# Kernel optimization log

Measured on AMD Instinct MI355X. Metric: run time of the kernel, lower is better.

Reference implementation:

```python
import jax, jax.numpy as jnp
import numpy as np

NUM_CLASSES = 150
EPS = 1e-8


def _class_centers(features, labels):
    # features: [B, Cf, H, W] float; labels: [B, H, W] int
    # Single-pass segment reduce over pixels keyed by class label, replacing the
    # original O(C*N) per-class masked passes.
    B, Cf, H, W = features.shape
    f = features.reshape(B, Cf, H * W)          # [B, Cf, N]
    l = labels.reshape(B, H * W)                # [B, N]

    def per_batch(fb, lb):
        # fb: [Cf, N], lb: [N]
        sums = jax.ops.segment_sum(fb.T, lb, num_segments=NUM_CLASSES)      # [C, Cf]
        counts = jax.ops.segment_sum(jnp.ones_like(lb, fb.dtype), lb,
                                      num_segments=NUM_CLASSES)             # [C]
        return sums / (counts[:, None] + EPS)                               # [C, Cf]

    centers = jax.vmap(per_batch)(f, l)         # [B, C, Cf]
    return centers.mean(axis=0)                 # [C, Cf]


def setup_inputs() -> dict:
    key = jax.random.key(0)
    k1, k2, k3, k4 = jax.random.split(key, 4)
    B, Cf, H, W = 1, 256, 512, 512
    return {
        "src_fea": jax.random.normal(k1, (B, Cf, H, W), dtype=jnp.float32),
        "trg_fea": jax.random.normal(k2, (B, Cf, H, W), dtype=jnp.float32),
        "src_labels": jax.random.randint(k3, (B, H, W), 0, NUM_CLASSES, dtype=jnp.int32),
        "trg_pseudo_labels": jax.random.randint(k4, (B, H, W), 0, NUM_CLASSES, dtype=jnp.int32),
    }


def reference(src_fea, trg_fea, src_labels, trg_pseudo_labels):
    cs = _class_centers(src_fea, src_labels)                # [C, Cf]
    ct = _class_centers(trg_fea, trg_pseudo_labels)         # [C, Cf]
    return jnp.linalg.norm(cs - ct)                         # scalar Frobenius norm
```

## Files before the change

kernel.cpp:

```cpp
#include <hip/hip_runtime.h>
#include <math.h>

#define N_PIX (512 * 512)
#define NQ (N_PIX / 4)
#define NUM_CLASSES 150
#define CF 256
#define ACC_STRIDE 151
#define DUMP 150
#define PIX_PER_BLOCK 2048
#define QUADS_PER_BLOCK (PIX_PER_BLOCK / 4)
#define CHUNKS (N_PIX / PIX_PER_BLOCK)
#define THREADS 256
#define EPS 1e-8f


__device__ __forceinline__ void rmw_quad(float* __restrict__ arow, float4 v,
                                         int4 L) {
  float vx = v.x, vy = v.y, vz = v.z, vw = v.w;
  int ax = L.x, ay = L.y, az = L.z, aw = L.w;
  if (L.y == L.x) { vx += vy; ay = DUMP; }
  if (L.z == L.x) { vx += vz; az = DUMP; }
  else if (L.z == L.y) { vy += vz; az = DUMP; }
  if (L.w == L.x) { vx += vw; aw = DUMP; }
  else if (L.w == L.y) { vy += vw; aw = DUMP; }
  else if (L.w == L.z) { vz += vw; aw = DUMP; }
  const float r0 = arow[ax];
  const float r1 = arow[ay];
  const float r2 = arow[az];
  const float r3 = arow[aw];
  arow[ax] = r0 + vx;
  arow[ay] = r1 + vy;
  arow[az] = r2 + vz;
  arow[aw] = r3 + vw;
}

__global__ __launch_bounds__(THREADS, 1) void scatter_kernel(
    const float* __restrict__ f_src, const float* __restrict__ f_trg,
    const int* __restrict__ l_src, const int* __restrict__ l_trg,
    float* __restrict__ sums, float* __restrict__ cnt) {
  const int tensor = blockIdx.z;
  const float* __restrict__ f = tensor ? f_trg : f_src;
  const int* __restrict__ lab = tensor ? l_trg : l_src;

  __shared__ float acc[CF * ACC_STRIDE];

  const int t = threadIdx.x;
  for (int i = t; i < CF * ACC_STRIDE; i += THREADS) acc[i] = 0.f;
  __syncthreads();

  const int q0 = blockIdx.x * QUADS_PER_BLOCK;
  const float4* __restrict__ fb4 = (const float4*)f + (size_t)t * NQ;
  const int4* __restrict__ lab4 = (const int4*)lab;
  float* __restrict__ arow = &acc[t * ACC_STRIDE];

  int my_count = 0;

  int q = q0;
  float4 a0 = fb4[q + 0], a1 = fb4[q + 1], a2 = fb4[q + 2], a3 = fb4[q + 3];
  int4 b0 = lab4[q + 0], b1 = lab4[q + 1], b2 = lab4[q + 2], b3 = lab4[q + 3];

  for (int j = 0; j < QUADS_PER_BLOCK; j += 4) {
    const float4 v0 = a0, v1 = a1, v2 = a2, v3 = a3;
    const int4 L0 = b0, L1 = b1, L2 = b2, L3 = b3;
    q = q0 + ((j + 4) & (QUADS_PER_BLOCK - 1));
    a0 = fb4[q + 0]; a1 = fb4[q + 1]; a2 = fb4[q + 2]; a3 = fb4[q + 3];
    b0 = lab4[q + 0]; b1 = lab4[q + 1]; b2 = lab4[q + 2]; b3 = lab4[q + 3];

    my_count += (L0.x == t) + (L0.y == t) + (L0.z == t) + (L0.w == t) +
                (L1.x == t) + (L1.y == t) + (L1.z == t) + (L1.w == t) +
                (L2.x == t) + (L2.y == t) + (L2.z == t) + (L2.w == t) +
                (L3.x == t) + (L3.y == t) + (L3.z == t) + (L3.w == t);

    rmw_quad(arow, v0, L0);
    rmw_quad(arow, v1, L1);
    rmw_quad(arow, v2, L2);
    rmw_quad(arow, v3, L3);
  }
  __syncthreads();

  float* __restrict__ out = sums + tensor * (NUM_CLASSES * CF);
  for (int i = t; i < NUM_CLASSES * CF; i += THREADS) {
    const int cls = i >> 8;
    const int ch = i & (CF - 1);
    unsafeAtomicAdd(&out[i], acc[ch * ACC_STRIDE + cls]);
  }
  if (t < NUM_CLASSES)
    unsafeAtomicAdd(&cnt[tensor * NUM_CLASSES + t], (float)my_count);
}

#define FTHREADS 1024
__global__ __launch_bounds__(FTHREADS) void finalize_kernel(
    const float* __restrict__ sums, const float* __restrict__ cnt,
    float* __restrict__ out) {
  const float* ss = sums;
  const float* st = sums + NUM_CLASSES * CF;
  const float* cs = cnt;
  const float* ct = cnt + NUM_CLASSES;
  float acc = 0.f;
  for (int i = threadIdx.x; i < NUM_CLASSES * CF; i += FTHREADS) {
    const int cls = i >> 8;
    const float d = ss[i] / (cs[cls] + EPS) - st[i] / (ct[cls] + EPS);
    acc += d * d;
  }
#pragma unroll
  for (int off = 32; off > 0; off >>= 1) acc += __shfl_down(acc, off, 64);
  __shared__ float red[FTHREADS / 64];
  const int lane = threadIdx.x & 63;
  const int wid = threadIdx.x >> 6;
  if (lane == 0) red[wid] = acc;
  __syncthreads();
  if (threadIdx.x == 0) {
    float tsum = 0.f;
#pragma unroll
    for (int w = 0; w < FTHREADS / 64; ++w) tsum += red[w];
    out[0] = sqrtf(tsum);
  }
}

extern "C" void kernel_launch(void* const* d_in, const int* in_sizes, int n_in,
                              void* d_out, int out_size, void* d_ws,
                              size_t ws_size, hipStream_t stream) {
  const float* f_src = (const float*)d_in[0];
  const float* f_trg = (const float*)d_in[1];
  const int* l_src = (const int*)d_in[2];
  const int* l_trg = (const int*)d_in[3];
  float* out = (float*)d_out;

  float* sums = (float*)d_ws;
  float* cnt = sums + 2 * NUM_CLASSES * CF;

  const size_t zero_bytes =
      (size_t)(2 * NUM_CLASSES * CF + 2 * NUM_CLASSES) * sizeof(float);
  hipMemsetAsync(d_ws, 0, zero_bytes, stream);

  hipLaunchKernelGGL(scatter_kernel, dim3(CHUNKS, 1, 2), dim3(THREADS), 0,
                     stream, f_src, f_trg, l_src, l_trg, sums, cnt);
  hipLaunchKernelGGL(finalize_kernel, dim3(1), dim3(FTHREADS), 0, stream, sums,
                     cnt, out);
}
```

Baseline: 615.4 us.

## Stage packed labels in shared memory and double-buffer deeper feature prefetch

Labels for the block are loaded once cooperatively, packed into bytes, and stored in shared memory instead of every thread re-reading the same int4 labels from global memory. Feature loads are now double-buffered in batches of 16 float4s per thread, which raises memory-level parallelism to hide global latency in the scatter loop. This costs more registers (32 float4 buffers) and a small extra LDS array, and packing assumes labels fit in 8 bits.

```diff
diff --git a/kernel.cpp b/kernel.cpp
--- a/kernel.cpp
+++ b/kernel.cpp
@@ -11,19 +11,20 @@
 #define QUADS_PER_BLOCK (PIX_PER_BLOCK / 4)
 #define CHUNKS (N_PIX / PIX_PER_BLOCK)
 #define THREADS 256
+#define BATCH 16
 #define EPS 1e-8f
 
 
 __device__ __forceinline__ void rmw_quad(float* __restrict__ arow, float4 v,
-                                         int4 L) {
+                                         int lx, int ly, int lz, int lw) {
   float vx = v.x, vy = v.y, vz = v.z, vw = v.w;
-  int ax = L.x, ay = L.y, az = L.z, aw = L.w;
-  if (L.y == L.x) { vx += vy; ay = DUMP; }
-  if (L.z == L.x) { vx += vz; az = DUMP; }
-  else if (L.z == L.y) { vy += vz; az = DUMP; }
-  if (L.w == L.x) { vx += vw; aw = DUMP; }
-  else if (L.w == L.y) { vy += vw; aw = DUMP; }
-  else if (L.w == L.z) { vz += vw; aw = DUMP; }
+  int ax = lx, ay = ly, az = lz, aw = lw;
+  if (ly == lx) { vx += vy; ay = DUMP; }
+  if (lz == lx) { vx += vz; az = DUMP; }
+  else if (lz == ly) { vy += vz; az = DUMP; }
+  if (lw == lx) { vx += vw; aw = DUMP; }
+  else if (lw == ly) { vy += vw; aw = DUMP; }
+  else if (lw == lz) { vz += vw; aw = DUMP; }
   const float r0 = arow[ax];
   const float r1 = arow[ay];
   const float r2 = arow[az];
@@ -43,39 +44,50 @@
   const int* __restrict__ lab = tensor ? l_trg : l_src;
 
   __shared__ float acc[CF * ACC_STRIDE];
+  __shared__ unsigned int slab[QUADS_PER_BLOCK];
 
   const int t = threadIdx.x;
+  const int q0 = blockIdx.x * QUADS_PER_BLOCK;
+  const int4* __restrict__ lab4 = (const int4*)lab;
+
   for (int i = t; i < CF * ACC_STRIDE; i += THREADS) acc[i] = 0.f;
+  for (int i = t; i < QUADS_PER_BLOCK; i += THREADS) {
+    const int4 L = lab4[q0 + i];
+    slab[i] = (unsigned)L.x | ((unsigned)L.y << 8) | ((unsigned)L.z << 16) |
+              ((unsigned)L.w << 24);
+  }
   __syncthreads();
 
-  const int q0 = blockIdx.x * QUADS_PER_BLOCK;
   const float4* __restrict__ fb4 = (const float4*)f + (size_t)t * NQ;
-  const int4* __restrict__ lab4 = (const int4*)lab;
   float* __restrict__ arow = &acc[t * ACC_STRIDE];
-
   int my_count = 0;
 
-  int q = q0;
-  float4 a0 = fb4[q + 0], a1 = fb4[q + 1], a2 = fb4[q + 2], a3 = fb4[q + 3];
-  int4 b0 = lab4[q + 0], b1 = lab4[q + 1], b2 = lab4[q + 2], b3 = lab4[q + 3];
+#define PROCESS(BUF, JBASE)                                                  \
+  _Pragma("unroll") for (int k = 0; k < BATCH; ++k) {                        \
+    const unsigned pl = slab[(JBASE) + k];       \
+    const int lx = pl & 255;                                                 \
+    const int ly = (pl >> 8) & 255;                                          \
+    const int lz = (pl >> 16) & 255;                                         \
+    const int lw = pl >> 24;                                                 \
+    my_count += (lx == t) + (ly == t) + (lz == t) + (lw == t);               \
+    rmw_quad(arow, BUF[k], lx, ly, lz, lw);                                  \
+  }
 
-  for (int j = 0; j < QUADS_PER_BLOCK; j += 4) {
-    const float4 v0 = a0, v1 = a1, v2 = a2, v3 = a3;
-    const int4 L0 = b0, L1 = b1, L2 = b2, L3 = b3;
-    q = q0 + ((j + 4) & (QUADS_PER_BLOCK - 1));
-    a0 = fb4[q + 0]; a1 = fb4[q + 1]; a2 = fb4[q + 2]; a3 = fb4[q + 3];
-    b0 = lab4[q + 0]; b1 = lab4[q + 1]; b2 = lab4[q + 2]; b3 = lab4[q + 3];
+  float4 bufA[BATCH], bufB[BATCH];
+#pragma unroll
+  for (int i = 0; i < BATCH; ++i) bufA[i] = fb4[q0 + i];
 
-    my_count += (L0.x == t) + (L0.y == t) + (L0.z == t) + (L0.w == t) +
-                (L1.x == t) + (L1.y == t) + (L1.z == t) + (L1.w == t) +
-                (L2.x == t) + (L2.y == t) + (L2.z == t) + (L2.w == t) +
-                (L3.x == t) + (L3.y == t) + (L3.z == t) + (L3.w == t);
-
-    rmw_quad(arow, v0, L0);
-    rmw_quad(arow, v1, L1);
-    rmw_quad(arow, v2, L2);
-    rmw_quad(arow, v3, L3);
+  for (int j = 0; j < QUADS_PER_BLOCK; j += 2 * BATCH) {
+#pragma unroll
+    for (int i = 0; i < BATCH; ++i)
+      bufB[i] = fb4[q0 + j + BATCH + i];
+    PROCESS(bufA, j)
+#pragma unroll
+    for (int i = 0; i < BATCH; ++i)
+      bufA[i] = fb4[q0 + ((j + 2 * BATCH + i) & (QUADS_PER_BLOCK - 1))];
+    PROCESS(bufB, j + BATCH)
   }
+#undef PROCESS
   __syncthreads();
 
   float* __restrict__ out = sums + tensor * (NUM_CLASSES * CF);
```

Result: faster. 597.0 us (-3.0%).
